# Optimization experiments

Hardware: AMD Instinct MI355X
Metric: run time of the kernel (lower is better)

Reference implementation:

```python
import jax, jax.numpy as jnp
import numpy as np

NUM_HEADS = 8
TOPK_RATIO = 0.1


def setup_inputs() -> dict:
    key = jax.random.key(0)
    ks = jax.random.split(key, 5)
    B, N, C = 1, 8192, 512
    S = 16              # num_frames
    K = 4               # clusters
    x = jax.random.normal(ks[0], (B, N, C), dtype=jnp.float32)
    w_qkv = jax.random.normal(ks[1], (3 * C, C), dtype=jnp.float32) * (C ** -0.5)
    b_qkv = jax.random.normal(ks[2], (3 * C,), dtype=jnp.float32) * 0.02
    w_proj = jax.random.normal(ks[3], (C, C), dtype=jnp.float32) * (C ** -0.5)
    b_proj = jax.random.normal(ks[4], (C,), dtype=jnp.float32) * 0.02
    keyframes = jnp.arange(K, dtype=jnp.int64 if jax.config.jax_enable_x64 else jnp.int32) * (S // K)  # [0,4,8,12]
    clusters = jnp.arange(S, dtype=keyframes.dtype).reshape(K, S // K)  # 4 clusters of 4 frames
    return {"x": x, "w_qkv": w_qkv, "b_qkv": b_qkv, "w_proj": w_proj,
            "b_proj": b_proj, "keyframes": keyframes, "clusters": clusters,
            "num_frames": S}


def _hierarchy_attn(q, k, v, keyframes, clusters, num_frames):
    # q,k,v: [B,H,N,D]
    B, H, N, D = q.shape
    scale = D ** -0.5
    tpf = N // num_frames                     # tokens per frame
    K = clusters.shape[0]
    tok = jnp.arange(tpf)
    # keyframe query token indices: [K*tpf]
    key_q_idx = (keyframes[:, None] * tpf + tok[None, :]).reshape(-1)
    q_proto = q[:, :, key_q_idx, :]           # [B,H,K*tpf,D]
    # proto attention scores vs all keys: [B,H,K*tpf,N]
    scores = jnp.einsum('bhqd,bhnd->bhqn', q_proto * scale, k)
    # aggregate per cluster (over batch, heads, keyframe tokens) -> [K,N]
    agg = scores.reshape(B, H, K, tpf, N).mean(axis=(0, 1, 3))
    topk_num = max(1, int(tpf * K * TOPK_RATIO))
    _, topk_idx = jax.lax.top_k(agg, topk_num)          # [K, T]
    # cluster query token indices: [K, M] with M = frames_per_cluster*tpf
    cluster_q_idx = (clusters[:, :, None] * tpf + tok[None, None, :]).reshape(K, -1)
    q_c = q[:, :, cluster_q_idx, :]           # [B,H,K,M,D]
    k_c = k[:, :, topk_idx, :]                # [B,H,K,T,D]
    v_c = v[:, :, topk_idx, :]                # [B,H,K,T,D]
    attn = jax.nn.softmax(jnp.einsum('bhkmd,bhktd->bhkmt', q_c * scale, k_c), axis=-1)
    x_c = jnp.einsum('bhkmt,bhktd->bhkmd', attn, v_c)   # [B,H,K,M,D]
    x_out = jnp.zeros_like(q)
    x_out = x_out.at[:, :, cluster_q_idx.reshape(-1), :].set(
        x_c.reshape(B, H, K * x_c.shape[3], D))
    return x_out


def reference(x, w_qkv, b_qkv, w_proj, b_proj, keyframes, clusters, num_frames):
    B, N, C = x.shape
    H = NUM_HEADS
    D = C // H
    qkv = (x @ w_qkv.T + b_qkv).reshape(B, N, 3, H, D)
    qkv = jnp.transpose(qkv, (2, 0, 3, 1, 4))           # [3,B,H,N,D]
    q, k, v = qkv[0], qkv[1], qkv[2]
    x_out = _hierarchy_attn(q, k, v, keyframes, clusters, num_frames)  # [B,H,N,D]
    x_out = jnp.transpose(x_out, (0, 2, 1, 3)).reshape(B, N, C)
    return x_out @ w_proj.T + b_proj
```

## Files before the change

kernel.cpp:

```cpp
#include <hip/hip_runtime.h>
#include <hip/hip_bf16.h>

#define N_TOK 8192
#define C_DIM 512
#define NH 8
#define DH 64
#define KCLUST 4
#define TPF 512
#define TOPK 204
#define KVPAD 256
#define MPC 2048

#define WS_WQH    0
#define WS_WPH    393216
#define WS_QHI    524288
#define WS_KC     2621440
#define WS_VC     2883584
#define WS_XAHI   3145728
#define WS_XBARP  5242880
#define WS_QBAR   5275648
#define WS_G      5277696
#define WS_AGG    5279744
#define WS_TOPK   5312512

using frag16 = __attribute__((ext_vector_type(8))) short;
using f32x4  = __attribute__((ext_vector_type(4))) float;

__device__ __forceinline__ unsigned short f2bf(float x) {
  unsigned u = __float_as_uint(x);
  return (unsigned short)((u + 0x7fffu + ((u >> 16) & 1u)) >> 16);
}
__device__ __forceinline__ float bf2f(unsigned short h) {
  return __uint_as_float(((unsigned)h) << 16);
}
__device__ __forceinline__ unsigned pkbf(float a, float b) {
  __hip_bfloat162 t = __float22bfloat162_rn(make_float2(a, b));
  return *reinterpret_cast<unsigned*>(&t);
}

__global__ __launch_bounds__(256) void prep_xbar(
    const float* __restrict__ x, const int* __restrict__ keyframes,
    float* __restrict__ xbarp) {
  const int b = blockIdx.x, tid = threadIdx.x;
  int kk = b >> 4, s = b & 15;
  int base = keyframes[kk] * TPF + s * 32;
  float a0 = 0.f, a1 = 0.f;
  for (int t = 0; t < 32; t++) {
    a0 += x[(size_t)(base + t) * C_DIM + tid];
    a1 += x[(size_t)(base + t) * C_DIM + tid + 256];
  }
  xbarp[(kk * 16 + s) * C_DIM + tid] = a0;
  xbarp[(kk * 16 + s) * C_DIM + tid + 256] = a1;
}

__global__ __launch_bounds__(256) void qbar_wide(
    const float* __restrict__ w_qkv, const float* __restrict__ b_qkv,
    const float* __restrict__ xbarp, float* __restrict__ qbar) {
  __shared__ float xs[C_DIM];
  const int b = blockIdx.x, tid = threadIdx.x;
  const int kk = b & 3, h = (b >> 2) & 7, dg = b >> 5;
  for (int i = tid; i < C_DIM; i += 256) {
    float a = 0.f;
    for (int s = 0; s < 16; s++) a += xbarp[(kk * 16 + s) * C_DIM + i];
    xs[i] = a * (1.f / 512.f);
  }
  __syncthreads();
  const int wave = tid >> 6, lane = tid & 63;
  const int og = wave * 2 + (lane >> 5), lt = lane & 31;
  const int d = dg * 8 + og;
  const float4* w4 =
      reinterpret_cast<const float4*>(w_qkv + (size_t)(h * 64 + d) * C_DIM + lt * 16);
  const float4* x4 = reinterpret_cast<const float4*>(&xs[lt * 16]);
  float a = 0.f;
#pragma unroll
  for (int q = 0; q < 4; q++) {
    float4 wv = w4[q], xv = x4[q];
    a += wv.x * xv.x + wv.y * xv.y + wv.z * xv.z + wv.w * xv.w;
  }
#pragma unroll
  for (int off = 16; off >= 1; off >>= 1) a += __shfl_xor(a, off);
  if (lt == 0) qbar[(h * 4 + kk) * 64 + d] = a + b_qkv[h * 64 + d];
}

__global__ __launch_bounds__(256) void g_wide(
    const float* __restrict__ w_qkv, const float* __restrict__ qbar,
    float* __restrict__ g) {
  __shared__ float qs[C_DIM];
  __shared__ float red[16][16];
  const int b = blockIdx.x, tid = threadIdx.x;
  const int kk = b >> 5, cs = b & 31;
  for (int i = tid; i < C_DIM; i += 256)
    qs[i] = qbar[((i >> 6) * 4 + kk) * 64 + (i & 63)];
  __syncthreads();
  const int jg = tid >> 4, cl = tid & 15;
  const int c = cs * 16 + cl;
  const float* wk = w_qkv + (size_t)C_DIM * C_DIM + c;
  float a = 0.f;
#pragma unroll 4
  for (int j = jg * 32; j < jg * 32 + 32; j++)
    a += qs[j] * wk[(size_t)j * C_DIM];
  red[jg][cl] = a;
  __syncthreads();
  if (tid < 16) {
    float s = red[0][tid];
#pragma unroll
    for (int q = 1; q < 16; q++) s += red[q][tid];
    g[kk * C_DIM + cs * 16 + tid] = s;
  }
}

__global__ __launch_bounds__(256) void agg_wcvt(
    const float* __restrict__ x, const float* __restrict__ g,
    float* __restrict__ agg, const float* __restrict__ w_qkv,
    const float* __restrict__ w_proj, unsigned short* __restrict__ wqh,
    unsigned short* __restrict__ wph) {
  __shared__ float gs[KCLUST][C_DIM];
  const int bid = blockIdx.x, tid = threadIdx.x;
  if (bid >= 2048) {
    int bx = bid - 2048;
    const float* src = (bx < 768) ? w_qkv : w_proj;
    unsigned short* dst = (bx < 768) ? wqh : wph;
    int i = ((bx < 768) ? bx : (bx - 768)) * 256 + tid;
    float4 v = reinterpret_cast<const float4*>(src)[i];
    reinterpret_cast<uint2*>(dst)[i] = make_uint2(pkbf(v.x, v.y), pkbf(v.z, v.w));
    return;
  }
  for (int i = tid; i < KCLUST * C_DIM; i += 256) gs[i >> 9][i & 511] = g[i];
  __syncthreads();
  int wave = tid >> 6, lane = tid & 63;
  int n = bid * 4 + wave;
  const float4* xp = reinterpret_cast<const float4*>(x + (size_t)n * C_DIM);
  float4 xa = xp[lane], xb = xp[lane + 64];
  float a[4];
#pragma unroll
  for (int kk = 0; kk < 4; kk++) {
    const float4* gpv = reinterpret_cast<const float4*>(&gs[kk][0]);
    float4 ga = gpv[lane], gb2 = gpv[lane + 64];
    a[kk] = xa.x * ga.x + xa.y * ga.y + xa.z * ga.z + xa.w * ga.w +
            xb.x * gb2.x + xb.y * gb2.y + xb.z * gb2.z + xb.w * gb2.w;
  }
#pragma unroll
  for (int off = 32; off >= 1; off >>= 1) {
    a[0] += __shfl_xor(a[0], off);
    a[1] += __shfl_xor(a[1], off);
    a[2] += __shfl_xor(a[2], off);
    a[3] += __shfl_xor(a[3], off);
  }
  if (lane == 0) {
    agg[0 * N_TOK + n] = a[0];
    agg[1 * N_TOK + n] = a[1];
    agg[2 * N_TOK + n] = a[2];
    agg[3 * N_TOK + n] = a[3];
  }
}

__device__ __forceinline__ int block_scan_incl(int v, int* wsum, int tid) {
  int lane = tid & 63, wv = tid >> 6;
#pragma unroll
  for (int off = 1; off < 64; off <<= 1) {
    int t = __shfl_up(v, off, 64);
    if (lane >= off) v += t;
  }
  if (lane == 63) wsum[wv] = v;
  __syncthreads();
  if (wv > 0) v += wsum[0];
  if (wv > 1) v += wsum[1];
  if (wv > 2) v += wsum[2];
  __syncthreads();
  return v;
}

__global__ __launch_bounds__(256) void topk_kernel(const float* __restrict__ agg,
                                                   int* __restrict__ topk) {
  __shared__ unsigned sk[N_TOK];
  __shared__ int hist[256];
  __shared__ int scn[256];
  __shared__ int wsum[4];
  __shared__ int sel_bin, sel_rem;
  int kk = blockIdx.x, tid = threadIdx.x;
  const float* row = agg + (size_t)kk * N_TOK;

  for (int i = tid; i < N_TOK; i += 256) {
    unsigned u = __float_as_uint(row[i]);
    sk[i] = (u & 0x80000000u) ? ~u : (u | 0x80000000u);
  }
  __syncthreads();

  unsigned prefix = 0;
  int remaining = TOPK;
#pragma unroll
  for (int rnd = 3; rnd >= 0; rnd--) {
    int shift = rnd * 8;
    hist[tid] = 0;
    __syncthreads();
    for (int i = tid; i < N_TOK; i += 256) {
      unsigned key = sk[i];
      bool in = (rnd == 3) || ((key >> (shift + 8)) == prefix);
      if (in) atomicAdd(&hist[(key >> shift) & 255], 1);
    }
    __syncthreads();
    int sv = block_scan_incl(hist[255 - tid], wsum, tid);
    scn[tid] = sv;
    __syncthreads();
    int b = tid;
    int cgt = (b == 255) ? 0 : scn[254 - b];
    if (cgt < remaining && remaining <= cgt + hist[b]) {
      sel_bin = b;
      sel_rem = remaining - cgt;
    }
    __syncthreads();
    prefix = (prefix << 8) | (unsigned)sel_bin;
    remaining = sel_rem;
    __syncthreads();
  }
  unsigned kth = prefix;

  int* out_row = topk + kk * TOPK;
  int base = tid * 32;

  int cA = 0;
  for (int i = 0; i < 32; i++) cA += (sk[base + i] > kth) ? 1 : 0;
  int sA = block_scan_incl(cA, wsum, tid);
  scn[tid] = sA;
  __syncthreads();
  int exclA = sA - cA;
  int G = scn[255];
  int p = exclA;
  for (int i = 0; i < 32; i++)
    if (sk[base + i] > kth) out_row[p++] = base + i;
  __syncthreads();

  int cB = 0;
  for (int i = 0; i < 32; i++) cB += (sk[base + i] == kth) ? 1 : 0;
  int sB = block_scan_incl(cB, wsum, tid);
  int exclB = sB - cB;
  int pos = G + exclB;
  for (int i = 0; i < 32; i++) {
    if (sk[base + i] == kth) {
      if (pos < TOPK) out_row[pos] = base + i;
      pos++;
    }
  }
}

#define APAN 1032
#define BUFS 8256
__global__ __launch_bounds__(256) void gemm_qkv2(
    const float* __restrict__ x, const unsigned short* __restrict__ Bhi,
    const float* __restrict__ bias, const int* __restrict__ topk,
    unsigned short* __restrict__ qhi, unsigned short* __restrict__ kc,
    unsigned short* __restrict__ vc) {
  __shared__ short pool[17408];
  const int tid = threadIdx.x;
  const int bid = blockIdx.x;
  const bool is_kv = bid >= 256;
  int j0, m0 = 0, kk = 0, mloc = 0;
  if (!is_kv) {
    const int grp = bid >> 5;
    const int rem = bid & 31;
    j0 = (rem >> 3) * 128;
    m0 = (grp * 8 + (rem & 7)) * 128;
  } else {
    const int b2 = bid - 256;
    kk = b2 >> 4;
    const int sub = b2 & 15;
    mloc = (sub >> 3) * 128;
    j0 = 512 + (sub & 7) * 128;
  }
  const int wave = tid >> 6, lane = tid & 63;
  const int wr = wave >> 1, wc = wave & 1;
  const int qd = lane >> 4, ln = lane & 15;

  const int r0 = tid >> 2, p0 = tid & 3;
  const int r1 = r0 + 64;
  const float4 *pA0, *pA1;
  if (!is_kv) {
    pA0 = reinterpret_cast<const float4*>(x + (size_t)(m0 + r0) * C_DIM) + p0 * 2;
    pA1 = reinterpret_cast<const float4*>(x + (size_t)(m0 + r1) * C_DIM) + p0 * 2;
  } else {
    int t0i = mloc + r0, t1i = mloc + r1;
    if (t0i > TOPK - 1) t0i = TOPK - 1;
    if (t1i > TOPK - 1) t1i = TOPK - 1;
    const int tok0 = topk[kk * TOPK + t0i];
    const int tok1 = topk[kk * TOPK + t1i];
    pA0 = reinterpret_cast<const float4*>(x + (size_t)tok0 * C_DIM) + p0 * 2;
    pA1 = reinterpret_cast<const float4*>(x + (size_t)tok1 * C_DIM) + p0 * 2;
  }
  const unsigned short* pB0 = Bhi + (size_t)(j0 + r0) * C_DIM + p0 * 8;
  const unsigned short* pB1 = Bhi + (size_t)(j0 + r1) * C_DIM + p0 * 8;

  f32x4 acc[4][4] = {};

  float4 fa[4];
  uint4 rb[2];
  fa[0] = pA0[0]; fa[1] = pA0[1];
  fa[2] = pA1[0]; fa[3] = pA1[1];
  rb[0] = *reinterpret_cast<const uint4*>(pB0);
  rb[1] = *reinterpret_cast<const uint4*>(pB1);

  {
    *reinterpret_cast<uint4*>(&pool[p0 * APAN + r0 * 8]) =
        make_uint4(pkbf(fa[0].x, fa[0].y), pkbf(fa[0].z, fa[0].w),
                   pkbf(fa[1].x, fa[1].y), pkbf(fa[1].z, fa[1].w));
    *reinterpret_cast<uint4*>(&pool[p0 * APAN + r1 * 8]) =
        make_uint4(pkbf(fa[2].x, fa[2].y), pkbf(fa[2].z, fa[2].w),
                   pkbf(fa[3].x, fa[3].y), pkbf(fa[3].z, fa[3].w));
    *reinterpret_cast<uint4*>(&pool[4 * APAN + p0 * APAN + r0 * 8]) = rb[0];
    *reinterpret_cast<uint4*>(&pool[4 * APAN + p0 * APAN + r1 * 8]) = rb[1];
  }
  __syncthreads();

  int cur = 0;
#pragma unroll
  for (int it = 0; it < 16; it++) {
    if (it < 15) {
      int k4 = (it + 1) * 8;
      fa[0] = pA0[k4]; fa[1] = pA0[k4 + 1];
      fa[2] = pA1[k4]; fa[3] = pA1[k4 + 1];
      rb[0] = *reinterpret_cast<const uint4*>(pB0 + (it + 1) * 32);
      rb[1] = *reinterpret_cast<const uint4*>(pB1 + (it + 1) * 32);
    }
    const int bb = cur * BUFS;
    frag16 a_h[4], b_h[4];
#pragma unroll
    for (int i = 0; i < 4; i++) {
      int row = wr * 64 + i * 16 + ln;
      a_h[i] = *reinterpret_cast<const frag16*>(&pool[bb + qd * APAN + row * 8]);
    }
#pragma unroll
    for (int j = 0; j < 4; j++) {
      int row = wc * 64 + j * 16 + ln;
      b_h[j] = *reinterpret_cast<const frag16*>(&pool[bb + 4 * APAN + qd * APAN + row * 8]);
    }
#pragma unroll
    for (int i = 0; i < 4; i++)
#pragma unroll
      for (int j = 0; j < 4; j++)
        acc[i][j] = __builtin_amdgcn_mfma_f32_16x16x32_bf16(a_h[i], b_h[j], acc[i][j], 0, 0, 0);

    if (it < 15) {
      const int nb = (cur ^ 1) * BUFS;
      *reinterpret_cast<uint4*>(&pool[nb + p0 * APAN + r0 * 8]) =
          make_uint4(pkbf(fa[0].x, fa[0].y), pkbf(fa[0].z, fa[0].w),
                     pkbf(fa[1].x, fa[1].y), pkbf(fa[1].z, fa[1].w));
      *reinterpret_cast<uint4*>(&pool[nb + p0 * APAN + r1 * 8]) =
          make_uint4(pkbf(fa[2].x, fa[2].y), pkbf(fa[2].z, fa[2].w),
                     pkbf(fa[3].x, fa[3].y), pkbf(fa[3].z, fa[3].w));
      *reinterpret_cast<uint4*>(&pool[nb + 4 * APAN + p0 * APAN + r0 * 8]) = rb[0];
      *reinterpret_cast<uint4*>(&pool[nb + 4 * APAN + p0 * APAN + r1 * 8]) = rb[1];
    }
    __syncthreads();
    cur ^= 1;
  }

  const int sel = j0 >> 9;
  const float qscale = (sel == 0) ? 0.125f : 1.0f;
  short* sh = pool;

#pragma unroll
  for (int i = 0; i < 4; i++)
#pragma unroll
    for (int j = 0; j < 4; j++) {
      int jcol = wc * 64 + j * 16 + ln;
      float bv = bias[j0 + jcol];
#pragma unroll
      for (int r = 0; r < 4; r++) {
        int mrow = wr * 64 + i * 16 + qd * 4 + r;
        sh[mrow * 136 + jcol] = (short)f2bf((acc[i][j][r] + bv) * qscale);
      }
    }
  __syncthreads();
  if (!is_kv) {
#pragma unroll
    for (int p = 0; p < 8; p++) {
      int u = tid + p * 256;
      int row = u >> 4, c = (u & 15) * 8;
      int hh = ((j0 + c) >> 6) & 7, d0 = c & 63;
      *reinterpret_cast<uint4*>(qhi + ((size_t)hh * N_TOK + m0 + row) * DH + d0) =
          *reinterpret_cast<const uint4*>(&sh[row * 136 + c]);
    }
  } else {
    unsigned short* dstc = (sel == 1) ? kc : vc;
#pragma unroll
    for (int p = 0; p < 8; p++) {
      int u = tid + p * 256;
      int row = u >> 4, c = (u & 15) * 8;
      int hh = ((j0 + c) >> 6) & 7, d0 = c & 63;
      *reinterpret_cast<uint4*>(
          dstc + (((size_t)kk * 8 + hh) * KVPAD + mloc + row) * DH + d0) =
          *reinterpret_cast<const uint4*>(&sh[row * 136 + c]);
    }
  }
}

__global__ __launch_bounds__(256) void flash_mfma(
    const unsigned short* __restrict__ qhi, const unsigned short* __restrict__ kc,
    const unsigned short* __restrict__ vc, const int* __restrict__ clusters,
    unsigned short* __restrict__ xahi) {
  __shared__ short Ks[64 * 72];
  __shared__ short Vs[64 * 72];
  __shared__ short Ps[128 * 72];
  const int tid = threadIdx.x;
  const int qb = blockIdx.x, kk = blockIdx.y, h = blockIdx.z;
  const int wave = tid >> 6, lane = tid & 63;
  const int ln = lane & 15, qd = lane >> 4;

  const int q_local0 = qb * 128;
  const int frame = clusters[kk * 4 + (q_local0 >> 9)];
  const int tokbase = frame * TPF + (q_local0 & 511);
  const size_t kvbase = ((size_t)kk * 8 + h) * KVPAD * DH;

  frag16 qa_h[2][2];
#pragma unroll
  for (int mt = 0; mt < 2; mt++) {
    const int tok_m = tokbase + wave * 32 + mt * 16 + ln;
    const unsigned short* qr_h = qhi + ((size_t)h * N_TOK + tok_m) * DH;
#pragma unroll
    for (int s = 0; s < 2; s++)
      qa_h[mt][s] = *reinterpret_cast<const frag16*>(qr_h + s * 32 + qd * 8);
  }

  f32x4 acc_o[2][4] = {};
  float lsum[2][4] = {};

  for (int t0 = 0; t0 < 192; t0 += 64) {
#pragma unroll
    for (int i = 0; i < 2; i++) {
      int u = tid + i * 256;
      int r = u >> 3, oct = u & 7;
      *reinterpret_cast<frag16*>(&Ks[r * 72 + oct * 8]) =
          *reinterpret_cast<const frag16*>(kc + kvbase + (size_t)(t0 + r) * DH + oct * 8);
    }
    {
      int tk = (tid & 15) * 4, td = (tid >> 4) * 4;
      uint2 w2[4];
#pragma unroll
      for (int i = 0; i < 4; i++)
        w2[i] = *reinterpret_cast<const uint2*>(vc + kvbase + (size_t)(t0 + tk + i) * DH + td);
#pragma unroll
      for (int dd = 0; dd < 4; dd++) {
        unsigned s0 = (dd < 2) ? (w2[0].x >> (16 * dd)) : (w2[0].y >> (16 * (dd - 2)));
        unsigned s1 = (dd < 2) ? (w2[1].x >> (16 * dd)) : (w2[1].y >> (16 * (dd - 2)));
        unsigned s2 = (dd < 2) ? (w2[2].x >> (16 * dd)) : (w2[2].y >> (16 * (dd - 2)));
        unsigned s3 = (dd < 2) ? (w2[3].x >> (16 * dd)) : (w2[3].y >> (16 * (dd - 2)));
        *reinterpret_cast<uint2*>(&Vs[(td + dd) * 72 + tk]) =
            make_uint2((s0 & 0xffffu) | (s1 << 16), (s2 & 0xffffu) | (s3 << 16));
      }
    }
    __syncthreads();

#pragma unroll
    for (int mt = 0; mt < 2; mt++) {
      f32x4 sacc[4] = {};
#pragma unroll
      for (int c = 0; c < 4; c++) {
#pragma unroll
        for (int s = 0; s < 2; s++) {
          frag16 bh = *reinterpret_cast<const frag16*>(&Ks[(c * 16 + ln) * 72 + s * 32 + qd * 8]);
          sacc[c] = __builtin_amdgcn_mfma_f32_16x16x32_bf16(qa_h[mt][s], bh, sacc[c], 0, 0, 0);
        }
      }
#pragma unroll
      for (int c = 0; c < 4; c++) {
#pragma unroll
        for (int r = 0; r < 4; r++) {
          float p = __expf(sacc[c][r]);
          lsum[mt][r] += p;
          Ps[(wave * 32 + mt * 16 + qd * 4 + r) * 72 + c * 16 + ln] = (short)f2bf(p);
        }
      }
    }

#pragma unroll
    for (int mt = 0; mt < 2; mt++)
#pragma unroll
      for (int s = 0; s < 2; s++) {
        frag16 pa = *reinterpret_cast<const frag16*>(
            &Ps[(wave * 32 + mt * 16 + ln) * 72 + s * 32 + qd * 8]);
#pragma unroll
        for (int dt = 0; dt < 4; dt++) {
          frag16 vb = *reinterpret_cast<const frag16*>(&Vs[(dt * 16 + ln) * 72 + s * 32 + qd * 8]);
          acc_o[mt][dt] = __builtin_amdgcn_mfma_f32_16x16x32_bf16(pa, vb, acc_o[mt][dt], 0, 0, 0);
        }
      }
    __syncthreads();
  }

  {
    const int t0 = 192;
#pragma unroll
    for (int i = 0; i < 2; i++) {
      int u = tid + i * 256;
      int r = u >> 3, oct = u & 7;
      *reinterpret_cast<frag16*>(&Ks[r * 72 + oct * 8]) =
          *reinterpret_cast<const frag16*>(kc + kvbase + (size_t)(t0 + r) * DH + oct * 8);
    }
    {
      int tk = (tid & 15) * 4, td = (tid >> 4) * 4;
      uint2 w2[4];
#pragma unroll
      for (int i = 0; i < 4; i++)
        w2[i] = *reinterpret_cast<const uint2*>(vc + kvbase + (size_t)(t0 + tk + i) * DH + td);
#pragma unroll
      for (int dd = 0; dd < 4; dd++) {
        unsigned s0 = (dd < 2) ? (w2[0].x >> (16 * dd)) : (w2[0].y >> (16 * (dd - 2)));
        unsigned s1 = (dd < 2) ? (w2[1].x >> (16 * dd)) : (w2[1].y >> (16 * (dd - 2)));
        unsigned s2 = (dd < 2) ? (w2[2].x >> (16 * dd)) : (w2[2].y >> (16 * (dd - 2)));
        unsigned s3 = (dd < 2) ? (w2[3].x >> (16 * dd)) : (w2[3].y >> (16 * (dd - 2)));
        *reinterpret_cast<uint2*>(&Vs[(td + dd) * 72 + tk]) =
            make_uint2((s0 & 0xffffu) | (s1 << 16), (s2 & 0xffffu) | (s3 << 16));
      }
    }
    __syncthreads();

#pragma unroll
    for (int mt = 0; mt < 2; mt++) {
      f32x4 sacc = {};
#pragma unroll
      for (int s = 0; s < 2; s++) {
        frag16 bh = *reinterpret_cast<const frag16*>(&Ks[ln * 72 + s * 32 + qd * 8]);
        sacc = __builtin_amdgcn_mfma_f32_16x16x32_bf16(qa_h[mt][s], bh, sacc, 0, 0, 0);
      }
#pragma unroll
      for (int r = 0; r < 4; r++) {
        float p = (ln < 12) ? __expf(sacc[r]) : 0.f;
        lsum[mt][r] += p;
        int prow = (wave * 32 + mt * 16 + qd * 4 + r) * 72;
        Ps[prow + ln] = (short)f2bf(p);
        Ps[prow + 16 + ln] = 0;
      }
    }

#pragma unroll
    for (int mt = 0; mt < 2; mt++) {
      frag16 pa = *reinterpret_cast<const frag16*>(
          &Ps[(wave * 32 + mt * 16 + ln) * 72 + qd * 8]);
#pragma unroll
      for (int dt = 0; dt < 4; dt++) {
        frag16 vb = *reinterpret_cast<const frag16*>(&Vs[(dt * 16 + ln) * 72 + qd * 8]);
        acc_o[mt][dt] = __builtin_amdgcn_mfma_f32_16x16x32_bf16(pa, vb, acc_o[mt][dt], 0, 0, 0);
      }
    }
  }

#pragma unroll
  for (int mt = 0; mt < 2; mt++)
#pragma unroll
    for (int r = 0; r < 4; r++) {
      float l = lsum[mt][r];
      l += __shfl_xor(l, 1);
      l += __shfl_xor(l, 2);
      l += __shfl_xor(l, 4);
      l += __shfl_xor(l, 8);
      lsum[mt][r] = 1.f / l;
    }

#pragma unroll
  for (int mt = 0; mt < 2; mt++)
#pragma unroll
    for (int dt = 0; dt < 4; dt++)
#pragma unroll
      for (int r = 0; r < 4; r++)
        Ps[(wave * 32 + mt * 16 + qd * 4 + r) * 72 + dt * 16 + ln] =
            (short)f2bf(acc_o[mt][dt][r] * lsum[mt][r]);
  __syncthreads();
#pragma unroll
  for (int p = 0; p < 4; p++) {
    int u = tid + p * 256;
    int row = u >> 3, c = (u & 7) * 8;
    *reinterpret_cast<uint4*>(xahi + (size_t)(tokbase + row) * C_DIM + h * DH + c) =
        *reinterpret_cast<const uint4*>(&Ps[row * 72 + c]);
  }
}

__global__ __launch_bounds__(256) void gemm_proj(
    const unsigned short* __restrict__ Ahi, const unsigned short* __restrict__ Bhi,
    const float* __restrict__ bias, float* __restrict__ out) {
  __shared__ short pool[12288];
  short* As = pool;
  short* Bs = pool + 4096;
  const int tid = threadIdx.x;
  const int bid = blockIdx.x;
  const int grp = bid / 32;
  const int rem = bid - grp * 32;
  const int jblk = rem >> 3;
  const int m_idx = grp * 8 + (rem & 7);
  const int j0 = jblk * 128;
  const int m0 = m_idx * 64;
  const int wave = tid >> 6, lane = tid & 63;
  const int rh = wave >> 1, ch = wave & 1;
  const int qd = lane >> 4, ln = lane & 15;

  const int arow = tid & 63, ap = tid >> 6;
  const int brow = tid & 127, bp = tid >> 7;
  const unsigned short* pA = Ahi + (size_t)(m0 + arow) * C_DIM + ap * 8;
  const unsigned short* pB0 = Bhi + (size_t)(j0 + brow) * C_DIM + bp * 8;
  const unsigned short* pB1 = pB0 + 16;

  f32x4 acc[2][4] = {};

  uint4 ra = *reinterpret_cast<const uint4*>(pA);
  uint4 rb0 = *reinterpret_cast<const uint4*>(pB0);
  uint4 rb1 = *reinterpret_cast<const uint4*>(pB1);
  *reinterpret_cast<uint4*>(&As[ap * 512 + arow * 8]) = ra;
  *reinterpret_cast<uint4*>(&Bs[bp * 1024 + brow * 8]) = rb0;
  *reinterpret_cast<uint4*>(&Bs[(bp + 2) * 1024 + brow * 8]) = rb1;
  __syncthreads();

  int cur = 0;
#pragma unroll
  for (int it = 0; it < 16; it++) {
    if (it < 15) {
      int k = (it + 1) * 32;
      ra = *reinterpret_cast<const uint4*>(pA + k);
      rb0 = *reinterpret_cast<const uint4*>(pB0 + k);
      rb1 = *reinterpret_cast<const uint4*>(pB1 + k);
    }
    frag16 a_h[2], b_h[4];
#pragma unroll
    for (int i = 0; i < 2; i++)
      a_h[i] = *reinterpret_cast<const frag16*>(&As[cur * 2048 + qd * 512 + (rh * 32 + i * 16 + ln) * 8]);
#pragma unroll
    for (int j = 0; j < 4; j++)
      b_h[j] = *reinterpret_cast<const frag16*>(&Bs[cur * 4096 + qd * 1024 + (ch * 64 + j * 16 + ln) * 8]);
#pragma unroll
    for (int i = 0; i < 2; i++)
#pragma unroll
      for (int j = 0; j < 4; j++)
        acc[i][j] = __builtin_amdgcn_mfma_f32_16x16x32_bf16(a_h[i], b_h[j], acc[i][j], 0, 0, 0);
    if (it < 15) {
      int nxt = cur ^ 1;
      *reinterpret_cast<uint4*>(&As[nxt * 2048 + ap * 512 + arow * 8]) = ra;
      *reinterpret_cast<uint4*>(&Bs[nxt * 4096 + bp * 1024 + brow * 8]) = rb0;
      *reinterpret_cast<uint4*>(&Bs[nxt * 4096 + (bp + 2) * 1024 + brow * 8]) = rb1;
      __syncthreads();
      cur = nxt;
    }
  }

  float* sh32 = reinterpret_cast<float*>(pool);
#pragma unroll
  for (int chp = 0; chp < 2; chp++) {
    __syncthreads();
    if (ch == chp) {
#pragma unroll
      for (int i = 0; i < 2; i++)
#pragma unroll
        for (int j = 0; j < 4; j++) {
          int jcol = j * 16 + ln;
          float bv = bias[j0 + chp * 64 + jcol];
#pragma unroll
          for (int r = 0; r < 4; r++)
            sh32[(rh * 32 + i * 16 + qd * 4 + r) * 68 + jcol] = acc[i][j][r] + bv;
        }
    }
    __syncthreads();
#pragma unroll
    for (int p = 0; p < 4; p++) {
      int u = tid + p * 256;
      int row = u >> 4, c4 = (u & 15) * 4;
      *reinterpret_cast<float4*>(out + (size_t)(m0 + row) * C_DIM + j0 + chp * 64 + c4) =
          *reinterpret_cast<const float4*>(&sh32[row * 68 + c4]);
    }
  }
}

extern "C" void kernel_launch(void* const* d_in, const int* in_sizes, int n_in,
                              void* d_out, int out_size, void* d_ws, size_t ws_size,
                              hipStream_t stream) {
  const float* x = (const float*)d_in[0];
  const float* w_qkv = (const float*)d_in[1];
  const float* b_qkv = (const float*)d_in[2];
  const float* w_proj = (const float*)d_in[3];
  const float* b_proj = (const float*)d_in[4];
  const int* keyframes = (const int*)d_in[5];
  const int* clusters = (const int*)d_in[6];
  float* out = (float*)d_out;
  float* ws = (float*)d_ws;

  unsigned short* wqh = (unsigned short*)(ws + WS_WQH);
  unsigned short* wph = (unsigned short*)(ws + WS_WPH);
  unsigned short* qhi = (unsigned short*)(ws + WS_QHI);
  unsigned short* kc = (unsigned short*)(ws + WS_KC);
  unsigned short* vc = (unsigned short*)(ws + WS_VC);
  unsigned short* xahi = (unsigned short*)(ws + WS_XAHI);
  float* xbarp = ws + WS_XBARP;
  float* qbar = ws + WS_QBAR;
  float* g = ws + WS_G;
  float* agg = ws + WS_AGG;
  int* topkp = (int*)(ws + WS_TOPK);

  prep_xbar<<<64, 256, 0, stream>>>(x, keyframes, xbarp);
  qbar_wide<<<256, 256, 0, stream>>>(w_qkv, b_qkv, xbarp, qbar);
  g_wide<<<128, 256, 0, stream>>>(w_qkv, qbar, g);
  agg_wcvt<<<3072, 256, 0, stream>>>(x, g, agg, w_qkv, w_proj, wqh, wph);
  topk_kernel<<<4, 256, 0, stream>>>(agg, topkp);
  gemm_qkv2<<<320, 256, 0, stream>>>(x, wqh, b_qkv, topkp, qhi, kc, vc);
  flash_mfma<<<dim3(MPC / 128, KCLUST, NH), 256, 0, stream>>>(
      qhi, kc, vc, clusters, xahi);
  gemm_proj<<<512, 256, 0, stream>>>(xahi, wph, b_proj, out);
}
```

Measured before the change: 174.2 us.

## Fuse top-k selection into the KV blocks of the QKV GEMM kernel

Drops the separate 4-block top-k kernel launch. Each of the 64 K/V blocks of the QKV GEMM now recomputes the radix-select top-k for its cluster in shared memory and gathers its token indices locally. This removes one launch and its serialization gap, along with the global round trip of the index list. The cost is that the top-k work is repeated 16 times per cluster, which lengthens the K/V blocks (possibly the critical path), and shared memory grows slightly.

```diff
diff --git a/kernel.cpp b/kernel.cpp
--- a/kernel.cpp
+++ b/kernel.cpp
@@ -170,87 +170,14 @@
   return v;
 }
 
-__global__ __launch_bounds__(256) void topk_kernel(const float* __restrict__ agg,
-                                                   int* __restrict__ topk) {
-  __shared__ unsigned sk[N_TOK];
-  __shared__ int hist[256];
-  __shared__ int scn[256];
-  __shared__ int wsum[4];
-  __shared__ int sel_bin, sel_rem;
-  int kk = blockIdx.x, tid = threadIdx.x;
-  const float* row = agg + (size_t)kk * N_TOK;
-
-  for (int i = tid; i < N_TOK; i += 256) {
-    unsigned u = __float_as_uint(row[i]);
-    sk[i] = (u & 0x80000000u) ? ~u : (u | 0x80000000u);
-  }
-  __syncthreads();
-
-  unsigned prefix = 0;
-  int remaining = TOPK;
-#pragma unroll
-  for (int rnd = 3; rnd >= 0; rnd--) {
-    int shift = rnd * 8;
-    hist[tid] = 0;
-    __syncthreads();
-    for (int i = tid; i < N_TOK; i += 256) {
-      unsigned key = sk[i];
-      bool in = (rnd == 3) || ((key >> (shift + 8)) == prefix);
-      if (in) atomicAdd(&hist[(key >> shift) & 255], 1);
-    }
-    __syncthreads();
-    int sv = block_scan_incl(hist[255 - tid], wsum, tid);
-    scn[tid] = sv;
-    __syncthreads();
-    int b = tid;
-    int cgt = (b == 255) ? 0 : scn[254 - b];
-    if (cgt < remaining && remaining <= cgt + hist[b]) {
-      sel_bin = b;
-      sel_rem = remaining - cgt;
-    }
-    __syncthreads();
-    prefix = (prefix << 8) | (unsigned)sel_bin;
-    remaining = sel_rem;
-    __syncthreads();
-  }
-  unsigned kth = prefix;
-
-  int* out_row = topk + kk * TOPK;
-  int base = tid * 32;
-
-  int cA = 0;
-  for (int i = 0; i < 32; i++) cA += (sk[base + i] > kth) ? 1 : 0;
-  int sA = block_scan_incl(cA, wsum, tid);
-  scn[tid] = sA;
-  __syncthreads();
-  int exclA = sA - cA;
-  int G = scn[255];
-  int p = exclA;
-  for (int i = 0; i < 32; i++)
-    if (sk[base + i] > kth) out_row[p++] = base + i;
-  __syncthreads();
-
-  int cB = 0;
-  for (int i = 0; i < 32; i++) cB += (sk[base + i] == kth) ? 1 : 0;
-  int sB = block_scan_incl(cB, wsum, tid);
-  int exclB = sB - cB;
-  int pos = G + exclB;
-  for (int i = 0; i < 32; i++) {
-    if (sk[base + i] == kth) {
-      if (pos < TOPK) out_row[pos] = base + i;
-      pos++;
-    }
-  }
-}
-
 #define APAN 1032
 #define BUFS 8256
 __global__ __launch_bounds__(256) void gemm_qkv2(
     const float* __restrict__ x, const unsigned short* __restrict__ Bhi,
-    const float* __restrict__ bias, const int* __restrict__ topk,
+    const float* __restrict__ bias, const float* __restrict__ agg,
     unsigned short* __restrict__ qhi, unsigned short* __restrict__ kc,
     unsigned short* __restrict__ vc) {
-  __shared__ short pool[17408];
+  __shared__ __align__(16) short pool[17828];
   const int tid = threadIdx.x;
   const int bid = blockIdx.x;
   const bool is_kv = bid >= 256;
@@ -278,11 +205,82 @@
     pA0 = reinterpret_cast<const float4*>(x + (size_t)(m0 + r0) * C_DIM) + p0 * 2;
     pA1 = reinterpret_cast<const float4*>(x + (size_t)(m0 + r1) * C_DIM) + p0 * 2;
   } else {
+    unsigned* sk = reinterpret_cast<unsigned*>(pool);
+    int* hist = reinterpret_cast<int*>(pool + 16384);
+    int* scn = reinterpret_cast<int*>(pool + 16896);
+    int* wsum = reinterpret_cast<int*>(pool + 17408);
+    int* selv = reinterpret_cast<int*>(pool + 17416);
+    int* idxl = reinterpret_cast<int*>(pool + 17420);
+    const float* row = agg + (size_t)kk * N_TOK;
+
+    for (int i = tid; i < N_TOK; i += 256) {
+      unsigned u = __float_as_uint(row[i]);
+      sk[i] = (u & 0x80000000u) ? ~u : (u | 0x80000000u);
+    }
+    __syncthreads();
+
+    unsigned prefix = 0;
+    int remaining = TOPK;
+#pragma unroll
+    for (int rnd = 3; rnd >= 0; rnd--) {
+      int shift = rnd * 8;
+      hist[tid] = 0;
+      __syncthreads();
+      for (int i = tid; i < N_TOK; i += 256) {
+        unsigned key = sk[i];
+        bool in = (rnd == 3) || ((key >> (shift + 8)) == prefix);
+        if (in) atomicAdd(&hist[(key >> shift) & 255], 1);
+      }
+      __syncthreads();
+      int sv = block_scan_incl(hist[255 - tid], wsum, tid);
+      scn[tid] = sv;
+      __syncthreads();
+      int b = tid;
+      int cgt = (b == 255) ? 0 : scn[254 - b];
+      if (cgt < remaining && remaining <= cgt + hist[b]) {
+        selv[0] = b;
+        selv[1] = remaining - cgt;
+      }
+      __syncthreads();
+      prefix = (prefix << 8) | (unsigned)selv[0];
+      remaining = selv[1];
+      __syncthreads();
+    }
+    unsigned kth = prefix;
+    int base = tid * 32;
+
+    int cA = 0;
+    for (int i = 0; i < 32; i++) cA += (sk[base + i] > kth) ? 1 : 0;
+    int sA = block_scan_incl(cA, wsum, tid);
+    scn[tid] = sA;
+    __syncthreads();
+    int exclA = sA - cA;
+    int G = scn[255];
+    int p = exclA;
+    for (int i = 0; i < 32; i++)
+      if (sk[base + i] > kth) idxl[p++] = base + i;
+    __syncthreads();
+
+    int cB = 0;
+    for (int i = 0; i < 32; i++) cB += (sk[base + i] == kth) ? 1 : 0;
+    int sB = block_scan_incl(cB, wsum, tid);
+    int exclB = sB - cB;
+    int pos = G + exclB;
+    for (int i = 0; i < 32; i++) {
+      if (sk[base + i] == kth) {
+        if (pos < TOPK) idxl[pos] = base + i;
+        pos++;
+      }
+    }
+    __syncthreads();
+
     int t0i = mloc + r0, t1i = mloc + r1;
     if (t0i > TOPK - 1) t0i = TOPK - 1;
     if (t1i > TOPK - 1) t1i = TOPK - 1;
-    const int tok0 = topk[kk * TOPK + t0i];
-    const int tok1 = topk[kk * TOPK + t1i];
+    const int tok0 = idxl[t0i];
+    const int tok1 = idxl[t1i];
+    __syncthreads();
+
     pA0 = reinterpret_cast<const float4*>(x + (size_t)tok0 * C_DIM) + p0 * 2;
     pA1 = reinterpret_cast<const float4*>(x + (size_t)tok1 * C_DIM) + p0 * 2;
   }
@@ -688,14 +686,12 @@
   float* qbar = ws + WS_QBAR;
   float* g = ws + WS_G;
   float* agg = ws + WS_AGG;
-  int* topkp = (int*)(ws + WS_TOPK);
 
   prep_xbar<<<64, 256, 0, stream>>>(x, keyframes, xbarp);
   qbar_wide<<<256, 256, 0, stream>>>(w_qkv, b_qkv, xbarp, qbar);
   g_wide<<<128, 256, 0, stream>>>(w_qkv, qbar, g);
   agg_wcvt<<<3072, 256, 0, stream>>>(x, g, agg, w_qkv, w_proj, wqh, wph);
-  topk_kernel<<<4, 256, 0, stream>>>(agg, topkp);
-  gemm_qkv2<<<320, 256, 0, stream>>>(x, wqh, b_qkv, topkp, qhi, kc, vc);
+  gemm_qkv2<<<320, 256, 0, stream>>>(x, wqh, b_qkv, agg, qhi, kc, vc);
   flash_mfma<<<dim3(MPC / 128, KCLUST, NH), 256, 0, stream>>>(
       qhi, kc, vc, clusters, xahi);
   gemm_proj<<<512, 256, 0, stream>>>(xahi, wph, b_proj, out);
```

Result: no change. 174.3 us (+0.1%).
